# Kernel optimization log

Hardware: AMD Instinct MI355X
Metric: run time of the kernel (lower is better)

## Reference

```python
import jax, jax.numpy as jnp
import numpy as np

B, DIM, SIZE, NF = 16, 192, 48, 8
C2 = DIM // 2 + 1            # channel-rfft length (97)
HID = int(0.25 * DIM)        # reweight Mlp hidden (48)
FS = SIZE // 2 + 1           # spatial rfft width (25)
EPS = 1e-5


def setup_inputs() -> dict:
    key = jax.random.key(0)
    ks = jax.random.split(key, 12)
    n = lambda i, shape, s=0.02: jax.random.normal(ks[i], shape, jnp.float32) * s
    return {
        "r": jax.random.normal(ks[0], (B, DIM, SIZE, SIZE), jnp.float32),
        "t": jax.random.normal(ks[1], (B, DIM, SIZE, SIZE), jnp.float32),
        # BatchNorm2d (eval mode, running stats mean=0, var=1): [bn_r; bn_t]
        "bn_g": jnp.ones((2, DIM), jnp.float32),
        "bn_b": jnp.zeros((2, DIM), jnp.float32),
        # conv_r / conv_t 1x1 (with bias)
        "crt_w": n(2, (2, DIM, DIM)),
        "crt_b": jnp.zeros((2, DIM), jnp.float32),
        # StarReLU scale/bias: [act_r, act_t, mlp.act]
        "star_s": jnp.ones((3,), jnp.float32),
        "star_b": jnp.zeros((3,), jnp.float32),
        # reweight Mlp (bias=False)
        "fc1_w": n(3, (HID, DIM)),
        "fc2_w": n(4, (NF * DIM, HID)),
        # complex_weights [size, filter_size, num_filters, 2]
        "cw": n(5, (SIZE, FS, NF, 2)),
        # channel-spectrum enhance nets [rc_a, rc_p, tc_a, tc_p], each conv1x1->lrelu->conv1x1
        "enh_w1": n(6, (4, C2, C2)), "enh_b1": jnp.zeros((4, C2), jnp.float32),
        "enh_w2": n(7, (4, C2, C2)), "enh_b2": jnp.zeros((4, C2), jnp.float32),
        # conv_phase_r / conv_phase_t, each conv1x1->lrelu->conv1x1
        "ph_w1": n(8, (2, DIM, DIM)), "ph_b1": jnp.zeros((2, DIM), jnp.float32),
        "ph_w2": n(9, (2, DIM, DIM)), "ph_b2": jnp.zeros((2, DIM), jnp.float32),
        # DwconvFFN: BN (eval) + depthwise 3x3 (no bias)
        "dwbn_g": jnp.ones((DIM,), jnp.float32),
        "dwbn_b": jnp.zeros((DIM,), jnp.float32),
        "dw_w": n(10, (DIM, 1, 3, 3)),
    }


def _leaky(x):
    return jnp.where(x >= 0, x, 0.1 * x)


def _c1(x, w, b):  # 1x1 conv, NCHW
    return jnp.einsum('bchw,oc->bohw', x, w) + b[None, :, None, None]


def _net(x, w1, b1, w2, b2):  # conv1x1 -> LeakyReLU(0.1) -> conv1x1
    return _c1(_leaky(_c1(x, w1, b1)), w2, b2)


def _star(x, s, b):  # StarReLU: s * relu(x)^2 + b
    return s * jnp.square(jnp.maximum(x, 0.0)) + b


def _bn(x, g, b):  # eval-mode BN with running mean=0, var=1
    return x * (g / jnp.sqrt(1.0 + EPS))[None, :, None, None] + b[None, :, None, None]


def _forward(r, t, bn_g, bn_b, crt_w, crt_b, star_s, star_b, fc1_w, fc2_w, cw,
             enh_w1, enh_b1, enh_w2, enh_b2, ph_w1, ph_b1, ph_w2, ph_b2,
             dwbn_g, dwbn_b, dw_w):
    Bsz, D, H, W = r.shape
    res_r, res_t = r, t
    r = _bn(r, bn_g[0], bn_b[0])
    t = _bn(t, bn_g[1], bn_b[1])
    x = r + t
    # routeing: Mlp(mean over HW) -> [B, NF, D] softmax over filters
    h = _star(x.mean((2, 3)) @ fc1_w.T, star_s[2], star_b[2])
    route = jax.nn.softmax((h @ fc2_w.T).reshape(Bsz, NF, D), axis=1)
    r = _star(_c1(r, crt_w[0], crt_b[0]), star_s[0], star_b[0])
    t = _star(_c1(t, crt_w[1], crt_b[1]), star_s[1], star_b[1])

    def branch(u, ia, ip, iph):
        u_fft = jnp.fft.rfft2(u, axes=(2, 3), norm='ortho')   # [B,D,H,FS]
        a = jnp.abs(u_fft)
        p = jnp.angle(u_fft)
        cf = jnp.fft.rfft(a, axis=1, norm='ortho')            # channel rfft -> [B,C2,H,FS]
        ca, cp = jnp.abs(cf), jnp.angle(cf)
        caE = _net(ca, enh_w1[ia], enh_b1[ia], enh_w2[ia], enh_b2[ia])
        cpE = _net(cp, enh_w1[ip], enh_b1[ip], enh_w2[ip], enh_b2[ip])
        comp = caE * jnp.cos(cpE) + 1j * (caE * jnp.sin(cpE))
        c = jnp.fft.irfft(comp, n=D, axis=1, norm='ortho')    # back to [B,D,H,FS]
        sc = c * a
        pE = _net(p, ph_w1[iph], ph_b1[iph], ph_w2[iph], ph_b2[iph])
        return sc * jnp.cos(pE) + 1j * (sc * jnp.sin(pE))

    rt_s = branch(r, 0, 1, 0) + branch(t, 2, 3, 1)            # [B,D,H,FS] complex
    weight = cw[..., 0] + 1j * cw[..., 1]                     # [H,FS,NF]
    weights = jnp.einsum('bfc,hwf->bchw', route.astype(jnp.complex64), weight)
    rt = jnp.fft.irfft2(rt_s * weights, s=(H, W), axes=(2, 3), norm='ortho')
    out_1 = rt + res_r + res_t
    y = _bn(out_1, dwbn_g, dwbn_b)
    y = jax.lax.conv_general_dilated(
        y, dw_w, (1, 1), 'SAME',
        dimension_numbers=('NCHW', 'OIHW', 'NCHW'), feature_group_count=D)
    return y + out_1


def reference(r, t, bn_g, bn_b, crt_w, crt_b, star_s, star_b, fc1_w, fc2_w, cw,
              enh_w1, enh_b1, enh_w2, enh_b2, ph_w1, ph_b1, ph_w2, ph_b2,
              dwbn_g, dwbn_b, dw_w):
    return _forward(r, t, bn_g, bn_b, crt_w, crt_b, star_s, star_b, fc1_w, fc2_w, cw,
                    enh_w1, enh_b1, enh_w2, enh_b2, ph_w1, ph_b1, ph_w2, ph_b2,
                    dwbn_g, dwbn_b, dw_w)
```

## Files before the change

kernel.cpp:

```cpp
#include <hip/hip_runtime.h>
#include <math.h>

constexpr int B_   = 16;
constexpr int D_   = 192;
constexpr int S_   = 48;
constexpr int NF_  = 8;
constexpr int C2_  = 97;
constexpr int HID_ = 48;
constexpr int FS_  = 25;
constexpr int HW_  = S_ * S_;
constexpr int HWF_ = S_ * FS_;
constexpr float EPS_ = 1e-5f;
constexpr double PI_D = 3.14159265358979323846;

__global__ __launch_bounds__(192) void k_prep(const float* __restrict__ crt_w,
                                              const float* __restrict__ crt_b,
                                              const float* __restrict__ bn_g,
                                              const float* __restrict__ bn_b,
                                              float* __restrict__ Weff,
                                              float* __restrict__ beff)
{
    int io = blockIdx.x;
    int c  = threadIdx.x;
    int i  = io / D_;
    float s  = bn_g[i * D_ + c] * rsqrtf(1.f + EPS_);
    float bb = bn_b[i * D_ + c];
    float w  = crt_w[(size_t)io * D_ + c];
    Weff[(size_t)io * D_ + c] = w * s;
    __shared__ float red[D_];
    red[c] = w * bb;
    __syncthreads();
    if (c == 0) {
        float acc = 0.f;
        for (int j = 0; j < D_; ++j) acc += red[j];
        int o = io % D_;
        beff[io] = crt_b[i * D_ + o] + acc;
    }
}

__global__ __launch_bounds__(256) void k_mean(const float* __restrict__ r,
                                              const float* __restrict__ t,
                                              const float* __restrict__ bn_g,
                                              const float* __restrict__ bn_b,
                                              float* __restrict__ xm)
{
    int bd = blockIdx.x;
    int d  = bd % D_;
    float sr = bn_g[d]      * rsqrtf(1.f + EPS_);
    float st = bn_g[D_ + d] * rsqrtf(1.f + EPS_);
    const float* rp = r + (size_t)bd * HW_;
    const float* tp = t + (size_t)bd * HW_;
    float acc = 0.f;
    for (int i = threadIdx.x; i < HW_; i += 256) acc += rp[i] * sr + tp[i] * st;
    __shared__ float red[256];
    red[threadIdx.x] = acc;
    __syncthreads();
    for (int off = 128; off > 0; off >>= 1) {
        if (threadIdx.x < off) red[threadIdx.x] += red[threadIdx.x + off];
        __syncthreads();
    }
    if (threadIdx.x == 0)
        xm[bd] = red[0] * (1.f / HW_) + bn_b[d] + bn_b[D_ + d];
}

__global__ __launch_bounds__(192) void k_route(const float* __restrict__ xm,
                                               const float* __restrict__ fc1,
                                               const float* __restrict__ fc2,
                                               const float* __restrict__ star_s,
                                               const float* __restrict__ star_b,
                                               float* __restrict__ route)
{
    int b = blockIdx.x;
    int tid = threadIdx.x;
    __shared__ float x[D_];
    __shared__ float h[HID_];
    x[tid] = xm[b * D_ + tid];
    __syncthreads();
    if (tid < HID_) {
        float a = 0.f;
        const float* wp = fc1 + (size_t)tid * D_;
        for (int c = 0; c < D_; ++c) a += x[c] * wp[c];
        float rl = fmaxf(a, 0.f);
        h[tid] = star_s[2] * rl * rl + star_b[2];
    }
    __syncthreads();
    float lg[NF_];
    for (int f = 0; f < NF_; ++f) {
        const float* wp = fc2 + ((size_t)f * D_ + tid) * HID_;
        float a = 0.f;
        for (int j = 0; j < HID_; ++j) a += h[j] * wp[j];
        lg[f] = a;
    }
    float m = lg[0];
    for (int f = 1; f < NF_; ++f) m = fmaxf(m, lg[f]);
    float ssum = 0.f;
    for (int f = 0; f < NF_; ++f) { lg[f] = expf(lg[f] - m); ssum += lg[f]; }
    float inv = 1.f / ssum;
    for (int f = 0; f < NF_; ++f)
        route[((size_t)b * NF_ + f) * D_ + tid] = lg[f] * inv;
}

__global__ __launch_bounds__(256) void k_gemm(const float* __restrict__ in,
                                              const float* __restrict__ W,
                                              const float* __restrict__ bias,
                                              float* __restrict__ outp,
                                              int Cin, int Cout, int HWl, int NB, int act,
                                              const float* __restrict__ ssp,
                                              const float* __restrict__ sbp, int sidx)
{
    const int n0 = blockIdx.x * 64;
    const int o0 = blockIdx.y * 64;
    const int tid = threadIdx.x;
    const int tx = tid % 16, ty = tid / 16;
    __shared__ float As[16][68];
    __shared__ float Bs[16][68];
    float acc[4][4] = {};
    const int Ntot = NB * HWl;

    const int akk = tid % 16, aoo0 = tid / 16;
    const int nn = tid % 64, kb = tid / 64;
    const int n = n0 + nn;
    const bool nok = n < Ntot;
    int bidx = 0, hw = 0;
    if (nok) { bidx = n / HWl; hw = n % HWl; }
    const float* bp = in + (size_t)bidx * Cin * HWl + hw;

    for (int k0 = 0; k0 < Cin; k0 += 16) {
        #pragma unroll
        for (int j = 0; j < 4; ++j) {
            int oo = aoo0 + 16 * j;
            int o  = o0 + oo;
            int k  = k0 + akk;
            As[akk][oo] = (o < Cout && k < Cin) ? W[(size_t)o * Cin + k] : 0.f;
        }
        #pragma unroll
        for (int j = 0; j < 4; ++j) {
            int kk = kb + 4 * j;
            int k  = k0 + kk;
            Bs[kk][nn] = (nok && k < Cin) ? bp[(size_t)k * HWl] : 0.f;
        }
        __syncthreads();
        #pragma unroll
        for (int kk = 0; kk < 16; ++kk) {
            float4 av = *reinterpret_cast<const float4*>(&As[kk][ty * 4]);
            float4 bv = *reinterpret_cast<const float4*>(&Bs[kk][tx * 4]);
            acc[0][0] += av.x * bv.x; acc[0][1] += av.x * bv.y; acc[0][2] += av.x * bv.z; acc[0][3] += av.x * bv.w;
            acc[1][0] += av.y * bv.x; acc[1][1] += av.y * bv.y; acc[1][2] += av.y * bv.z; acc[1][3] += av.y * bv.w;
            acc[2][0] += av.z * bv.x; acc[2][1] += av.z * bv.y; acc[2][2] += av.z * bv.z; acc[2][3] += av.z * bv.w;
            acc[3][0] += av.w * bv.x; acc[3][1] += av.w * bv.y; acc[3][2] += av.w * bv.z; acc[3][3] += av.w * bv.w;
        }
        __syncthreads();
    }

    float ss = 0.f, sb = 0.f;
    if (act == 2) { ss = ssp[sidx]; sb = sbp[sidx]; }
    #pragma unroll
    for (int i = 0; i < 4; ++i) {
        int o = o0 + ty * 4 + i;
        if (o >= Cout) continue;
        float bs = bias[o];
        #pragma unroll
        for (int j = 0; j < 4; ++j) {
            int nj = n0 + tx * 4 + j;
            if (nj >= Ntot) continue;
            float v = acc[i][j] + bs;
            if (act == 1)      v = v >= 0.f ? v : 0.1f * v;
            else if (act == 2) { float rl = fmaxf(v, 0.f); v = ss * rl * rl + sb; }
            int bb = nj / HWl, hh = nj % HWl;
            outp[((size_t)bb * Cout + o) * HWl + hh] = v;
        }
    }
}

__global__ __launch_bounds__(256) void k_rfft2(const float* __restrict__ u,
                                               float* __restrict__ A,
                                               float* __restrict__ P)
{
    int bd = blockIdx.x;
    __shared__ float tu[HW_];
    __shared__ float rre[HWF_], rim[HWF_];
    __shared__ float tc[S_], ts[S_];
    int t = threadIdx.x;
    if (t < S_) { double ang = -2.0 * PI_D * (double)t / (double)S_; tc[t] = (float)cos(ang); ts[t] = (float)sin(ang); }
    for (int i = t; i < HW_; i += 256) tu[i] = u[(size_t)bd * HW_ + i];
    __syncthreads();
    for (int i = t; i < HWF_; i += 256) {
        int h = i / FS_, k = i % FS_;
        float ar = 0.f, ai = 0.f;
        int m = 0;
        for (int w = 0; w < S_; ++w) {
            float v = tu[h * S_ + w];
            ar += v * tc[m]; ai += v * ts[m];
            m += k; if (m >= S_) m -= S_;
        }
        rre[i] = ar; rim[i] = ai;
    }
    __syncthreads();
    for (int i = t; i < HWF_; i += 256) {
        int kh = i / FS_, w = i % FS_;
        float ar = 0.f, ai = 0.f;
        int m = 0;
        for (int h = 0; h < S_; ++h) {
            float xr = rre[h * FS_ + w], xi = rim[h * FS_ + w];
            float c = tc[m], s = ts[m];
            ar += xr * c - xi * s;
            ai += xr * s + xi * c;
            m += kh; if (m >= S_) m -= S_;
        }
        ar *= (1.f / 48.f); ai *= (1.f / 48.f);
        A[(size_t)bd * HWF_ + i] = sqrtf(ar * ar + ai * ai);
        P[(size_t)bd * HWF_ + i] = atan2f(ai, ar);
    }
}

__global__ __launch_bounds__(256) void k_chfft(const float* __restrict__ A,
                                               float* __restrict__ CA,
                                               float* __restrict__ CP)
{
    int bh = blockIdx.x;
    int b = bh / S_, h = bh % S_;
    __shared__ float ta[D_ * FS_];
    __shared__ float tc[D_], ts[D_];
    int t = threadIdx.x;
    for (int i = t; i < D_; i += 256) {
        double ang = -2.0 * PI_D * (double)i / (double)D_;
        tc[i] = (float)cos(ang); ts[i] = (float)sin(ang);
    }
    for (int i = t; i < D_ * FS_; i += 256) {
        int d = i / FS_, w = i % FS_;
        ta[i] = A[(((size_t)b * D_ + d) * S_ + h) * FS_ + w];
    }
    __syncthreads();
    const float nrm = rsqrtf((float)D_);
    for (int i = t; i < C2_ * FS_; i += 256) {
        int k = i / FS_, w = i % FS_;
        float ar = 0.f, ai = 0.f;
        int m = 0;
        for (int d = 0; d < D_; ++d) {
            float v = ta[d * FS_ + w];
            ar += v * tc[m]; ai += v * ts[m];
            m += k; if (m >= D_) m -= D_;
        }
        ar *= nrm; ai *= nrm;
        size_t o = (((size_t)b * C2_ + k) * S_ + h) * FS_ + w;
        CA[o] = sqrtf(ar * ar + ai * ai);
        CP[o] = atan2f(ai, ar);
    }
}

__global__ __launch_bounds__(256) void k_chirfft(const float* __restrict__ CAe,
                                                 const float* __restrict__ CPe,
                                                 float* __restrict__ Asc)
{
    int bh = blockIdx.x;
    int b = bh / S_, h = bh % S_;
    __shared__ float Ar[C2_ * FS_], Ai[C2_ * FS_];
    __shared__ float tc[D_], ts[D_];
    int t = threadIdx.x;
    for (int i = t; i < D_; i += 256) {
        double ang = 2.0 * PI_D * (double)i / (double)D_;
        tc[i] = (float)cos(ang); ts[i] = (float)sin(ang);
    }
    for (int i = t; i < C2_ * FS_; i += 256) {
        int k = i / FS_, w = i % FS_;
        size_t o = (((size_t)b * C2_ + k) * S_ + h) * FS_ + w;
        float amp = CAe[o], ph = CPe[o];
        float sn, cs; sincosf(ph, &sn, &cs);
        Ar[i] = amp * cs; Ai[i] = amp * sn;
    }
    __syncthreads();
    const float nrm = rsqrtf((float)D_);
    for (int i = t; i < D_ * FS_; i += 256) {
        int d = i / FS_, w = i % FS_;
        float acc = Ar[w] + ((d & 1) ? -1.f : 1.f) * Ar[(C2_ - 1) * FS_ + w];
        float s2 = 0.f;
        int m = d;
        for (int k = 1; k < C2_ - 1; ++k) {
            s2 += Ar[k * FS_ + w] * tc[m] - Ai[k * FS_ + w] * ts[m];
            m += d; if (m >= D_) m -= D_;
        }
        float c = (acc + 2.f * s2) * nrm;
        size_t o = (((size_t)b * D_ + d) * S_ + h) * FS_ + w;
        Asc[o] = c * Asc[o];
    }
}

__global__ __launch_bounds__(256) void k_combine(const float* __restrict__ sc,
                                                 const float* __restrict__ pe,
                                                 float* __restrict__ rre,
                                                 float* __restrict__ rim, int addf)
{
    size_t n = (size_t)B_ * D_ * HWF_;
    for (size_t i = (size_t)blockIdx.x * 256 + threadIdx.x; i < n; i += (size_t)gridDim.x * 256) {
        float s = sc[i], p = pe[i];
        float sn, cs; sincosf(p, &sn, &cs);
        float re = s * cs, im = s * sn;
        if (addf) { rre[i] += re; rim[i] += im; }
        else      { rre[i]  = re; rim[i]  = im; }
    }
}

__global__ __launch_bounds__(256) void k_final(const float* __restrict__ rre,
                                               const float* __restrict__ rim,
                                               const float* __restrict__ route,
                                               const float* __restrict__ cw,
                                               const float* __restrict__ rin,
                                               const float* __restrict__ tin,
                                               float* __restrict__ out1)
{
    int bd = blockIdx.x;
    int b = bd / D_, d = bd % D_;
    __shared__ float sRe[HWF_], sIm[HWF_];
    __shared__ float cRe[HWF_], cIm[HWF_];
    __shared__ float tc[S_], ts[S_];
    __shared__ float rt[NF_];
    int t = threadIdx.x;
    if (t < S_) { double ang = 2.0 * PI_D * (double)t / (double)S_; tc[t] = (float)cos(ang); ts[t] = (float)sin(ang); }
    if (t < NF_) rt[t] = route[((size_t)b * NF_ + t) * D_ + d];
    __syncthreads();
    for (int i = t; i < HWF_; i += 256) {
        const float* cwp = cw + (size_t)i * NF_ * 2;
        float wr = 0.f, wi = 0.f;
        #pragma unroll
        for (int f = 0; f < NF_; ++f) { wr += rt[f] * cwp[2 * f]; wi += rt[f] * cwp[2 * f + 1]; }
        float xr = rre[(size_t)bd * HWF_ + i], xi = rim[(size_t)bd * HWF_ + i];
        sRe[i] = xr * wr - xi * wi;
        sIm[i] = xr * wi + xi * wr;
    }
    __syncthreads();
    for (int i = t; i < HWF_; i += 256) {
        int hp = i / FS_, w = i % FS_;
        float ar = 0.f, ai = 0.f;
        int m = 0;
        for (int h = 0; h < S_; ++h) {
            float xr = sRe[h * FS_ + w], xi = sIm[h * FS_ + w];
            ar += xr * tc[m] - xi * ts[m];
            ai += xr * ts[m] + xi * tc[m];
            m += hp; if (m >= S_) m -= S_;
        }
        cRe[i] = ar; cIm[i] = ai;
    }
    __syncthreads();
    for (int i = t; i < HW_; i += 256) {
        int hp = i / S_, n = i % S_;
        float acc = cRe[hp * FS_] + ((n & 1) ? -1.f : 1.f) * cRe[hp * FS_ + FS_ - 1];
        float s2 = 0.f;
        int m = n;
        for (int k = 1; k < FS_ - 1; ++k) {
            s2 += cRe[hp * FS_ + k] * tc[m] - cIm[hp * FS_ + k] * ts[m];
            m += n; if (m >= S_) m -= S_;
        }
        float v = (acc + 2.f * s2) * (1.f / 48.f);
        size_t o = (size_t)bd * HW_ + i;
        out1[o] = v + rin[o] + tin[o];
    }
}

__global__ __launch_bounds__(256) void k_dw(const float* __restrict__ out1,
                                            const float* __restrict__ g,
                                            const float* __restrict__ bbn,
                                            const float* __restrict__ wdw,
                                            float* __restrict__ outp)
{
    int bd = blockIdx.x;
    int d = bd % D_;
    __shared__ float tile[HW_];
    int t = threadIdx.x;
    for (int i = t; i < HW_; i += 256) tile[i] = out1[(size_t)bd * HW_ + i];
    float sc = g[d] * rsqrtf(1.f + EPS_);
    float bb = bbn[d];
    float w9[9];
    #pragma unroll
    for (int q = 0; q < 9; ++q) w9[q] = wdw[d * 9 + q];
    __syncthreads();
    for (int i = t; i < HW_; i += 256) {
        int y = i / S_, x = i % S_;
        float acc = 0.f;
        #pragma unroll
        for (int ki = 0; ki < 3; ++ki) {
            int yy = y + ki - 1;
            if (yy < 0 || yy >= S_) continue;
            #pragma unroll
            for (int kj = 0; kj < 3; ++kj) {
                int xx = x + kj - 1;
                if (xx < 0 || xx >= S_) continue;
                acc += w9[ki * 3 + kj] * (tile[yy * S_ + xx] * sc + bb);
            }
        }
        outp[(size_t)bd * HW_ + i] = acc + tile[i];
    }
}

extern "C" void kernel_launch(void* const* d_in, const int* in_sizes, int n_in,
                              void* d_out, int out_size, void* d_ws, size_t ws_size,
                              hipStream_t stream)
{
    (void)in_sizes; (void)n_in; (void)out_size; (void)ws_size;
    const float* r      = (const float*)d_in[0];
    const float* t      = (const float*)d_in[1];
    const float* bn_g   = (const float*)d_in[2];
    const float* bn_b   = (const float*)d_in[3];
    const float* crt_w  = (const float*)d_in[4];
    const float* crt_b  = (const float*)d_in[5];
    const float* star_s = (const float*)d_in[6];
    const float* star_b = (const float*)d_in[7];
    const float* fc1_w  = (const float*)d_in[8];
    const float* fc2_w  = (const float*)d_in[9];
    const float* cw     = (const float*)d_in[10];
    const float* enh_w1 = (const float*)d_in[11];
    const float* enh_b1 = (const float*)d_in[12];
    const float* enh_w2 = (const float*)d_in[13];
    const float* enh_b2 = (const float*)d_in[14];
    const float* ph_w1  = (const float*)d_in[15];
    const float* ph_b1  = (const float*)d_in[16];
    const float* ph_w2  = (const float*)d_in[17];
    const float* ph_b2  = (const float*)d_in[18];
    const float* dwbn_g = (const float*)d_in[19];
    const float* dwbn_b = (const float*)d_in[20];
    const float* dw_w   = (const float*)d_in[21];
    float* out = (float*)d_out;

    float* ws = (float*)d_ws;
    size_t off = 0;
    float* UACT = ws + off; off += (size_t)B_ * D_ * HW_;
    float* A_   = ws + off; off += (size_t)B_ * D_ * HWF_;
    float* P_   = ws + off; off += (size_t)B_ * D_ * HWF_;
    float* RRE  = ws + off; off += (size_t)B_ * D_ * HWF_;
    float* RIM  = ws + off; off += (size_t)B_ * D_ * HWF_;
    float* CA   = ws + off; off += (size_t)B_ * C2_ * HWF_;
    float* CP   = ws + off; off += (size_t)B_ * C2_ * HWF_;
    float* CH   = ws + off; off += (size_t)B_ * C2_ * HWF_;
    float* XM   = ws + off; off += B_ * D_;
    float* ROUTE= ws + off; off += B_ * NF_ * D_;
    float* WEFF = ws + off; off += 2 * D_ * D_;
    float* BEFF = ws + off; off += 2 * D_;
    float* HT   = UACT;

    k_prep<<<2 * D_, D_, 0, stream>>>(crt_w, crt_b, bn_g, bn_b, WEFF, BEFF);
    k_mean<<<B_ * D_, 256, 0, stream>>>(r, t, bn_g, bn_b, XM);
    k_route<<<B_, D_, 0, stream>>>(XM, fc1_w, fc2_w, star_s, star_b, ROUTE);

    for (int br = 0; br < 2; ++br) {
        const float* u_in = (br == 0) ? r : t;
        const int ia = (br == 0) ? 0 : 2;
        const int ip = (br == 0) ? 1 : 3;
        const int iph = br;

        k_gemm<<<dim3(576, 3), 256, 0, stream>>>(u_in, WEFF + (size_t)br * D_ * D_, BEFF + br * D_,
                                                 UACT, D_, D_, HW_, B_, 2, star_s, star_b, br);
        k_rfft2<<<B_ * D_, 256, 0, stream>>>(UACT, A_, P_);
        k_chfft<<<B_ * S_, 256, 0, stream>>>(A_, CA, CP);
        k_gemm<<<dim3(300, 2), 256, 0, stream>>>(CA, enh_w1 + (size_t)ia * C2_ * C2_, enh_b1 + ia * C2_,
                                                 CH, C2_, C2_, HWF_, B_, 1, nullptr, nullptr, 0);
        k_gemm<<<dim3(300, 2), 256, 0, stream>>>(CH, enh_w2 + (size_t)ia * C2_ * C2_, enh_b2 + ia * C2_,
                                                 CA, C2_, C2_, HWF_, B_, 0, nullptr, nullptr, 0);
        k_gemm<<<dim3(300, 2), 256, 0, stream>>>(CP, enh_w1 + (size_t)ip * C2_ * C2_, enh_b1 + ip * C2_,
                                                 CH, C2_, C2_, HWF_, B_, 1, nullptr, nullptr, 0);
        k_gemm<<<dim3(300, 2), 256, 0, stream>>>(CH, enh_w2 + (size_t)ip * C2_ * C2_, enh_b2 + ip * C2_,
                                                 CP, C2_, C2_, HWF_, B_, 0, nullptr, nullptr, 0);
        k_chirfft<<<B_ * S_, 256, 0, stream>>>(CA, CP, A_);
        k_gemm<<<dim3(300, 3), 256, 0, stream>>>(P_, ph_w1 + (size_t)iph * D_ * D_, ph_b1 + iph * D_,
                                                 HT, D_, D_, HWF_, B_, 1, nullptr, nullptr, 0);
        k_gemm<<<dim3(300, 3), 256, 0, stream>>>(HT, ph_w2 + (size_t)iph * D_ * D_, ph_b2 + iph * D_,
                                                 P_, D_, D_, HWF_, B_, 0, nullptr, nullptr, 0);
        k_combine<<<2048, 256, 0, stream>>>(A_, P_, RRE, RIM, br);
    }

    k_final<<<B_ * D_, 256, 0, stream>>>(RRE, RIM, ROUTE, cw, r, t, UACT);
    k_dw<<<B_ * D_, 256, 0, stream>>>(UACT, dwbn_g, dwbn_b, dw_w, out);
}
```

Measured before the change: 1.406 ms.

## Widen GEMM tiles, batch enhance GEMMs via grid z, fuse combine into epilogue

The GEMM tile grows from 64x64 to 64x128 with a 4x8 per-thread micro-tile, which raises reuse of data held in shared memory. The amplitude and phase enhance GEMMs now run as one batched launch along blockIdx.z with stride arguments, which halves the number of launches. The separate sincos combine kernel is removed: the second phase GEMM's epilogue computes the polar-to-complex result and accumulates it into zero-initialised RRE/RIM with atomicAdd. In exchange it adds a memset, more register pressure and atomic traffic.

```diff
diff --git a/kernel.cpp b/kernel.cpp
--- a/kernel.cpp
+++ b/kernel.cpp
@@ -106,19 +106,30 @@
                                               float* __restrict__ outp,
                                               int Cin, int Cout, int HWl, int NB, int act,
                                               const float* __restrict__ ssp,
-                                              const float* __restrict__ sbp, int sidx)
-{
-    const int n0 = blockIdx.x * 64;
+                                              const float* __restrict__ sbp, int sidx,
+                                              long instr, long wstr, long bstr, long ostr,
+                                              const float* __restrict__ scp,
+                                              float* __restrict__ rre,
+                                              float* __restrict__ rim)
+{
+    const int z = blockIdx.z;
+    in   += (long)z * instr;
+    W    += (long)z * wstr;
+    bias += (long)z * bstr;
+    outp += (long)z * ostr;
+
+    const int n0 = blockIdx.x * 128;
     const int o0 = blockIdx.y * 64;
     const int tid = threadIdx.x;
-    const int tx = tid % 16, ty = tid / 16;
-    __shared__ float As[16][68];
-    __shared__ float Bs[16][68];
-    float acc[4][4] = {};
+    const int tx = tid & 15;
+    const int ty = tid >> 4;
+    __shared__ float As[16][72];
+    __shared__ float Bs[16][136];
+    float acc[4][8] = {};
     const int Ntot = NB * HWl;
 
-    const int akk = tid % 16, aoo0 = tid / 16;
-    const int nn = tid % 64, kb = tid / 64;
+    const int akk = tid & 15, aoo0 = tid >> 4;
+    const int nn = tid & 127, kb = tid >> 7;
     const int n = n0 + nn;
     const bool nok = n < Ntot;
     int bidx = 0, hw = 0;
@@ -134,8 +145,8 @@
             As[akk][oo] = (o < Cout && k < Cin) ? W[(size_t)o * Cin + k] : 0.f;
         }
         #pragma unroll
-        for (int j = 0; j < 4; ++j) {
-            int kk = kb + 4 * j;
+        for (int j = 0; j < 8; ++j) {
+            int kk = kb * 8 + j;
             int k  = k0 + kk;
             Bs[kk][nn] = (nok && k < Cin) ? bp[(size_t)k * HWl] : 0.f;
         }
@@ -143,11 +154,15 @@
         #pragma unroll
         for (int kk = 0; kk < 16; ++kk) {
             float4 av = *reinterpret_cast<const float4*>(&As[kk][ty * 4]);
-            float4 bv = *reinterpret_cast<const float4*>(&Bs[kk][tx * 4]);
-            acc[0][0] += av.x * bv.x; acc[0][1] += av.x * bv.y; acc[0][2] += av.x * bv.z; acc[0][3] += av.x * bv.w;
-            acc[1][0] += av.y * bv.x; acc[1][1] += av.y * bv.y; acc[1][2] += av.y * bv.z; acc[1][3] += av.y * bv.w;
-            acc[2][0] += av.z * bv.x; acc[2][1] += av.z * bv.y; acc[2][2] += av.z * bv.z; acc[2][3] += av.z * bv.w;
-            acc[3][0] += av.w * bv.x; acc[3][1] += av.w * bv.y; acc[3][2] += av.w * bv.z; acc[3][3] += av.w * bv.w;
+            float4 b0 = *reinterpret_cast<const float4*>(&Bs[kk][tx * 8]);
+            float4 b1 = *reinterpret_cast<const float4*>(&Bs[kk][tx * 8 + 4]);
+            float a4[4] = {av.x, av.y, av.z, av.w};
+            float b8[8] = {b0.x, b0.y, b0.z, b0.w, b1.x, b1.y, b1.z, b1.w};
+            #pragma unroll
+            for (int i = 0; i < 4; ++i)
+                #pragma unroll
+                for (int j = 0; j < 8; ++j)
+                    acc[i][j] += a4[i] * b8[j];
         }
         __syncthreads();
     }
@@ -160,14 +175,22 @@
         if (o >= Cout) continue;
         float bs = bias[o];
         #pragma unroll
-        for (int j = 0; j < 4; ++j) {
-            int nj = n0 + tx * 4 + j;
+        for (int j = 0; j < 8; ++j) {
+            int nj = n0 + tx * 8 + j;
             if (nj >= Ntot) continue;
             float v = acc[i][j] + bs;
-            if (act == 1)      v = v >= 0.f ? v : 0.1f * v;
-            else if (act == 2) { float rl = fmaxf(v, 0.f); v = ss * rl * rl + sb; }
             int bb = nj / HWl, hh = nj % HWl;
-            outp[((size_t)bb * Cout + o) * HWl + hh] = v;
+            size_t oi = ((size_t)bb * Cout + o) * HWl + hh;
+            if (act == 3) {
+                float s = scp[oi];
+                float sn, cs; sincosf(v, &sn, &cs);
+                atomicAdd(&rre[oi], s * cs);
+                atomicAdd(&rim[oi], s * sn);
+            } else {
+                if (act == 1)      v = v >= 0.f ? v : 0.1f * v;
+                else if (act == 2) { float rl = fmaxf(v, 0.f); v = ss * rl * rl + sb; }
+                outp[oi] = v;
+            }
         }
     }
 }
@@ -282,21 +305,6 @@
         float c = (acc + 2.f * s2) * nrm;
         size_t o = (((size_t)b * D_ + d) * S_ + h) * FS_ + w;
         Asc[o] = c * Asc[o];
-    }
-}
-
-__global__ __launch_bounds__(256) void k_combine(const float* __restrict__ sc,
-                                                 const float* __restrict__ pe,
-                                                 float* __restrict__ rre,
-                                                 float* __restrict__ rim, int addf)
-{
-    size_t n = (size_t)B_ * D_ * HWF_;
-    for (size_t i = (size_t)blockIdx.x * 256 + threadIdx.x; i < n; i += (size_t)gridDim.x * 256) {
-        float s = sc[i], p = pe[i];
-        float sn, cs; sincosf(p, &sn, &cs);
-        float re = s * cs, im = s * sn;
-        if (addf) { rre[i] += re; rim[i] += im; }
-        else      { rre[i]  = re; rim[i]  = im; }
     }
 }
 
@@ -420,21 +428,25 @@
     const float* dw_w   = (const float*)d_in[21];
     float* out = (float*)d_out;
 
+    const long NDHWF = (long)B_ * D_ * HWF_;
+    const long SLOTC = (long)B_ * C2_ * HWF_;
+
     float* ws = (float*)d_ws;
     size_t off = 0;
     float* UACT = ws + off; off += (size_t)B_ * D_ * HW_;
-    float* A_   = ws + off; off += (size_t)B_ * D_ * HWF_;
-    float* P_   = ws + off; off += (size_t)B_ * D_ * HWF_;
-    float* RRE  = ws + off; off += (size_t)B_ * D_ * HWF_;
-    float* RIM  = ws + off; off += (size_t)B_ * D_ * HWF_;
-    float* CA   = ws + off; off += (size_t)B_ * C2_ * HWF_;
-    float* CP   = ws + off; off += (size_t)B_ * C2_ * HWF_;
-    float* CH   = ws + off; off += (size_t)B_ * C2_ * HWF_;
+    float* A_   = ws + off; off += NDHWF;
+    float* P_   = ws + off; off += NDHWF;
+    float* RRE  = ws + off; off += NDHWF;
+    float* RIM  = ws + off; off += NDHWF;
+    float* CA2  = ws + off; off += 2 * SLOTC;
     float* XM   = ws + off; off += B_ * D_;
     float* ROUTE= ws + off; off += B_ * NF_ * D_;
     float* WEFF = ws + off; off += 2 * D_ * D_;
     float* BEFF = ws + off; off += 2 * D_;
+    float* CH   = UACT;
     float* HT   = UACT;
+
+    hipMemsetAsync(RRE, 0, (size_t)(2 * NDHWF) * sizeof(float), stream);
 
     k_prep<<<2 * D_, D_, 0, stream>>>(crt_w, crt_b, bn_g, bn_b, WEFF, BEFF);
     k_mean<<<B_ * D_, 256, 0, stream>>>(r, t, bn_g, bn_b, XM);
@@ -443,27 +455,22 @@
     for (int br = 0; br < 2; ++br) {
         const float* u_in = (br == 0) ? r : t;
         const int ia = (br == 0) ? 0 : 2;
-        const int ip = (br == 0) ? 1 : 3;
-        const int iph = br;
-
-        k_gemm<<<dim3(576, 3), 256, 0, stream>>>(u_in, WEFF + (size_t)br * D_ * D_, BEFF + br * D_,
-                                                 UACT, D_, D_, HW_, B_, 2, star_s, star_b, br);
+
+        k_gemm<<<dim3(288, 3, 1), 256, 0, stream>>>(u_in, WEFF + (size_t)br * D_ * D_, BEFF + br * D_,
+            UACT, D_, D_, HW_, B_, 2, star_s, star_b, br, 0, 0, 0, 0, nullptr, nullptr, nullptr);
         k_rfft2<<<B_ * D_, 256, 0, stream>>>(UACT, A_, P_);
-        k_chfft<<<B_ * S_, 256, 0, stream>>>(A_, CA, CP);
-        k_gemm<<<dim3(300, 2), 256, 0, stream>>>(CA, enh_w1 + (size_t)ia * C2_ * C2_, enh_b1 + ia * C2_,
-                                                 CH, C2_, C2_, HWF_, B_, 1, nullptr, nullptr, 0);
-        k_gemm<<<dim3(300, 2), 256, 0, stream>>>(CH, enh_w2 + (size_t)ia * C2_ * C2_, enh_b2 + ia * C2_,
-                                                 CA, C2_, C2_, HWF_, B_, 0, nullptr, nullptr, 0);
-        k_gemm<<<dim3(300, 2), 256, 0, stream>>>(CP, enh_w1 + (size_t)ip * C2_ * C2_, enh_b1 + ip * C2_,
-                                                 CH, C2_, C2_, HWF_, B_, 1, nullptr, nullptr, 0);
-        k_gemm<<<dim3(300, 2), 256, 0, stream>>>(CH, enh_w2 + (size_t)ip * C2_ * C2_, enh_b2 + ip * C2_,
-                                                 CP, C2_, C2_, HWF_, B_, 0, nullptr, nullptr, 0);
-        k_chirfft<<<B_ * S_, 256, 0, stream>>>(CA, CP, A_);
-        k_gemm<<<dim3(300, 3), 256, 0, stream>>>(P_, ph_w1 + (size_t)iph * D_ * D_, ph_b1 + iph * D_,
-                                                 HT, D_, D_, HWF_, B_, 1, nullptr, nullptr, 0);
-        k_gemm<<<dim3(300, 3), 256, 0, stream>>>(HT, ph_w2 + (size_t)iph * D_ * D_, ph_b2 + iph * D_,
-                                                 P_, D_, D_, HWF_, B_, 0, nullptr, nullptr, 0);
-        k_combine<<<2048, 256, 0, stream>>>(A_, P_, RRE, RIM, br);
+        k_chfft<<<B_ * S_, 256, 0, stream>>>(A_, CA2, CA2 + SLOTC);
+        k_gemm<<<dim3(150, 2, 2), 256, 0, stream>>>(CA2, enh_w1 + (size_t)ia * C2_ * C2_, enh_b1 + ia * C2_,
+            CH, C2_, C2_, HWF_, B_, 1, nullptr, nullptr, 0,
+            SLOTC, (long)C2_ * C2_, C2_, SLOTC, nullptr, nullptr, nullptr);
+        k_gemm<<<dim3(150, 2, 2), 256, 0, stream>>>(CH, enh_w2 + (size_t)ia * C2_ * C2_, enh_b2 + ia * C2_,
+            CA2, C2_, C2_, HWF_, B_, 0, nullptr, nullptr, 0,
+            SLOTC, (long)C2_ * C2_, C2_, SLOTC, nullptr, nullptr, nullptr);
+        k_chirfft<<<B_ * S_, 256, 0, stream>>>(CA2, CA2 + SLOTC, A_);
+        k_gemm<<<dim3(150, 3, 1), 256, 0, stream>>>(P_, ph_w1 + (size_t)br * D_ * D_, ph_b1 + br * D_,
+            HT, D_, D_, HWF_, B_, 1, nullptr, nullptr, 0, 0, 0, 0, 0, nullptr, nullptr, nullptr);
+        k_gemm<<<dim3(150, 3, 1), 256, 0, stream>>>(HT, ph_w2 + (size_t)br * D_ * D_, ph_b2 + br * D_,
+            P_, D_, D_, HWF_, B_, 3, nullptr, nullptr, 0, 0, 0, 0, 0, A_, RRE, RIM);
     }
 
     k_final<<<B_ * D_, 256, 0, stream>>>(RRE, RIM, ROUTE, cw, r, t, UACT);
```

Result: slower. 1.800 ms (+28.0%).
